# Kernel tuning notes

Hardware: AMD Instinct MI355X
Metric: run time of the kernel (lower is better)

Reference implementation:

```python
import jax, jax.numpy as jnp
import numpy as np

N_NODES = 40000
N_EDGES = 640000
D = 128
N_GRAPHS = 64


def gcn_conv(x, W, b, edge_index):
    """PyG-style GCNConv: add self-loops, symmetric norm, linear, scatter-add."""
    n = x.shape[0]
    loops = jnp.arange(n, dtype=edge_index.dtype)
    src = jnp.concatenate([edge_index[0], loops])  # message sources (x_j)
    dst = jnp.concatenate([edge_index[1], loops])  # aggregation targets
    # deg computed over targets (col) with unit edge weights, incl. self-loops
    deg = jax.ops.segment_sum(jnp.ones_like(src, dtype=x.dtype), dst, num_segments=n)
    dinv = jnp.where(deg > 0, jax.lax.rsqrt(jnp.maximum(deg, 1.0)), 0.0)
    norm = dinv[src] * dinv[dst]  # [E+N]
    h = x @ W  # [N, d_out]
    out = jax.ops.segment_sum(norm[:, None] * h[src], dst, num_segments=n)
    return out + b


def global_mean_pool(x, batch, num_graphs):
    summed = jax.ops.segment_sum(x, batch, num_segments=num_graphs)
    counts = jax.ops.segment_sum(jnp.ones((x.shape[0],), x.dtype), batch, num_segments=num_graphs)
    return summed / jnp.maximum(counts, 1.0)[:, None]


def setup_inputs() -> dict:
    key = jax.random.key(0)
    ks = jax.random.split(key, 6)
    x = jax.random.normal(ks[0], (N_NODES, D), dtype=jnp.float32)
    edge_index = jax.random.randint(ks[1], (2, N_EDGES), 0, N_NODES)
    batch = jnp.sort(jax.random.randint(ks[2], (N_NODES,), 0, N_GRAPHS))
    s = 1.0 / np.sqrt(D)
    W1 = jax.random.normal(ks[3], (D, D), dtype=jnp.float32) * s
    W2 = jax.random.normal(ks[4], (D, D), dtype=jnp.float32) * s
    b1 = jnp.zeros((D,), jnp.float32)
    b2 = jnp.zeros((D,), jnp.float32)
    return {"x": x, "edge_index": edge_index, "batch": batch,
            "W1": W1, "b1": b1, "W2": W2, "b2": b2}


def reference(x, edge_index, batch, W1, b1, W2, b2):
    h = jax.nn.relu(gcn_conv(x, W1, b1, edge_index))
    h = gcn_conv(h, W2, b2, edge_index)  # no ReLU on last layer
    return global_mean_pool(h, batch, N_GRAPHS)
```

## Files before the change

kernel.cpp:

```cpp
#include <hip/hip_runtime.h>

#define D 128
#define N_GRAPHS 64

typedef unsigned int uint32;
typedef __attribute__((ext_vector_type(8))) _Float16 f16x8;
typedef __attribute__((ext_vector_type(4))) float f32x4;

__device__ __forceinline__ float hl(uint32 u) {
    return (float)__builtin_bit_cast(_Float16, (unsigned short)(u & 0xFFFF));
}
__device__ __forceinline__ float hh(uint32 u) {
    return (float)__builtin_bit_cast(_Float16, (unsigned short)(u >> 16));
}
__device__ __forceinline__ uint32 h2pair(float a, float b) {
    unsigned short ua = __builtin_bit_cast(unsigned short, (_Float16)a);
    unsigned short ub = __builtin_bit_cast(unsigned short, (_Float16)b);
    return (uint32)ua | ((uint32)ub << 16);
}

__global__ __launch_bounds__(256) void prep_kernel(int* __restrict__ cnt,
                                                   const float* __restrict__ W1,
                                                   uint32* __restrict__ Wh, int n) {
    int i = blockIdx.x * 256 + threadIdx.x;
    if (i < n) {
        cnt[i] = 0;
    } else if (i < n + D * (D / 2)) {
        int j = i - n;
        int nn = j & 127, kd = j >> 7;
        float v0 = W1[(size_t)(2 * kd) * D + nn];
        float v1 = W1[(size_t)(2 * kd + 1) * D + nn];
        Wh[nn * 64 + kd] = h2pair(v0, v1);
    }
}


#define GBM 64

__global__ __launch_bounds__(256) void count_gemm_kernel(
    const float* __restrict__ A, const uint32* __restrict__ Wh,
    uint32* __restrict__ hb, int M, int gemmBlocks,
    const int* __restrict__ dst, int* __restrict__ cnt,
    int* __restrict__ rank, int E) {
    __shared__ uint32 lds[64 * 68];

    if (blockIdx.x >= gemmBlocks) {
        int e = (blockIdx.x - gemmBlocks) * 256 + threadIdx.x;
        if (e < E) rank[e] = atomicAdd(&cnt[dst[e]], 1);
        return;
    }

    uint32* As = lds;
    int tid = threadIdx.x;
    int row0 = blockIdx.x * GBM;

#pragma unroll
    for (int j = 0; j < 8; ++j) {
        int idx = tid + j * 256;
        int r = idx >> 5, c4 = idx & 31;
        float4 v = make_float4(0.f, 0.f, 0.f, 0.f);
        if (row0 + r < M) v = *(const float4*)&A[(size_t)(row0 + r) * D + c4 * 4];
        As[r * 68 + c4 * 2 + 0] = h2pair(v.x, v.y);
        As[r * 68 + c4 * 2 + 1] = h2pair(v.z, v.w);
    }
    __syncthreads();

    int wave = tid >> 6, lane = tid & 63;
    int quad = lane >> 4, l16 = lane & 15;
    int wr = (wave & 1) * 32;
    int wc = (wave >> 1) * 64;
    f32x4 acc[2][4];
#pragma unroll
    for (int mi = 0; mi < 2; ++mi)
#pragma unroll
        for (int ni = 0; ni < 4; ++ni) acc[mi][ni] = (f32x4){0.f, 0.f, 0.f, 0.f};

#pragma unroll
    for (int ks = 0; ks < 4; ++ks) {
        int kd = ks * 16 + quad * 4;
        f16x8 a0 = *(f16x8*)&As[(wr + l16) * 68 + kd];
        f16x8 a1 = *(f16x8*)&As[(wr + 16 + l16) * 68 + kd];
        f16x8 b0 = *(const f16x8*)&Wh[(wc + l16) * 64 + kd];
        f16x8 b1 = *(const f16x8*)&Wh[(wc + 16 + l16) * 64 + kd];
        f16x8 b2 = *(const f16x8*)&Wh[(wc + 32 + l16) * 64 + kd];
        f16x8 b3 = *(const f16x8*)&Wh[(wc + 48 + l16) * 64 + kd];
        acc[0][0] = __builtin_amdgcn_mfma_f32_16x16x32_f16(a0, b0, acc[0][0], 0, 0, 0);
        acc[0][1] = __builtin_amdgcn_mfma_f32_16x16x32_f16(a0, b1, acc[0][1], 0, 0, 0);
        acc[0][2] = __builtin_amdgcn_mfma_f32_16x16x32_f16(a0, b2, acc[0][2], 0, 0, 0);
        acc[0][3] = __builtin_amdgcn_mfma_f32_16x16x32_f16(a0, b3, acc[0][3], 0, 0, 0);
        acc[1][0] = __builtin_amdgcn_mfma_f32_16x16x32_f16(a1, b0, acc[1][0], 0, 0, 0);
        acc[1][1] = __builtin_amdgcn_mfma_f32_16x16x32_f16(a1, b1, acc[1][1], 0, 0, 0);
        acc[1][2] = __builtin_amdgcn_mfma_f32_16x16x32_f16(a1, b2, acc[1][2], 0, 0, 0);
        acc[1][3] = __builtin_amdgcn_mfma_f32_16x16x32_f16(a1, b3, acc[1][3], 0, 0, 0);
    }
    __syncthreads();

    unsigned short* cs = (unsigned short*)lds;
#pragma unroll
    for (int mi = 0; mi < 2; ++mi)
#pragma unroll
        for (int ni = 0; ni < 4; ++ni)
#pragma unroll
            for (int r = 0; r < 4; ++r) {
                int row = wr + mi * 16 + quad * 4 + r;
                int col2 = wc + ni * 16 + l16;
                cs[row * 128 + col2] =
                    __builtin_bit_cast(unsigned short, (_Float16)acc[mi][ni][r]);
            }
    __syncthreads();
#pragma unroll
    for (int j = 0; j < 4; ++j) {
        int idx = tid + j * 256;
        int r = idx >> 4, q = idx & 15;
        if (row0 + r < M)
            *(uint4*)&hb[(size_t)(row0 + r) * 64 + q * 4] = *(uint4*)&lds[r * 64 + q * 4];
    }
}


__global__ __launch_bounds__(1024) void scanA_kernel(const int* __restrict__ cnt,
                                                     int* __restrict__ rowptr,
                                                     int* __restrict__ tot,
                                                     float* __restrict__ dinv, int n) {
    __shared__ int swave[16];
    int t = threadIdx.x;
    int lane = t & 63, wave = t >> 6;
    int i = blockIdx.x * 1024 + t;
    int orig = (i < n) ? cnt[i] : 0;
    int v = orig;
#pragma unroll
    for (int off = 1; off < 64; off <<= 1) {
        int u = __shfl_up(v, off, 64);
        if (lane >= off) v += u;
    }
    if (lane == 63) swave[wave] = v;
    __syncthreads();
    if (wave == 0) {
        int wv = (lane < 16) ? swave[lane] : 0;
#pragma unroll
        for (int off = 1; off < 16; off <<= 1) {
            int u = __shfl_up(wv, off, 64);
            if (lane >= off) wv += u;
        }
        if (lane < 16) swave[lane] = wv;
    }
    if (i < n) dinv[i] = rsqrtf((float)(orig + 1));
    __syncthreads();
    int incl = v + ((wave > 0) ? swave[wave - 1] : 0);
    if (i < n) rowptr[i] = incl - orig;
    if (t == 1023) tot[blockIdx.x] = incl;
}

__global__ __launch_bounds__(1024) void scanB_kernel(int* __restrict__ rowptr,
                                                     const int* __restrict__ tot,
                                                     int n, int nchunks) {
    __shared__ int soff;
    int b = blockIdx.x, t = threadIdx.x;
    if (t == 0) {
        int o = 0;
        for (int j = 0; j < b; ++j) o += tot[j];
        soff = o;
    }
    __syncthreads();
    int i = b * 1024 + t;
    if (i < n) rowptr[i] += soff;
    if (b == 0 && t == 0) {
        int o = 0;
        for (int j = 0; j < nchunks; ++j) o += tot[j];
        rowptr[n] = o;
    }
}

__global__ void fill_kernel(const int* __restrict__ src, const int* __restrict__ dst,
                            const int* __restrict__ rowptr, const int* __restrict__ rank,
                            int* __restrict__ col, int E) {
    int e = blockIdx.x * blockDim.x + threadIdx.x;
    if (e < E) col[rowptr[dst[e]] + rank[e]] = src[e];
}


__global__ __launch_bounds__(128) void agg_kernel(const uint32* __restrict__ hb,
                                                  const int* __restrict__ rowptr,
                                                  const int* __restrict__ col,
                                                  const float* __restrict__ dinv,
                                                  const float* __restrict__ bias,
                                                  uint32* __restrict__ h1, int n) {
    int tid = threadIdx.x;
    int lane32 = tid & 31;
    int slot = tid >> 5;
    int node = blockIdx.x * 4 + slot;
    if (node >= n) return;
    const uint2* __restrict__ h2 = (const uint2*)hb;

    float di = dinv[node];
    float ws = di * di;
    uint2 su = h2[(size_t)node * 32 + lane32];
    float a0 = ws * hl(su.x), a1 = ws * hh(su.x);
    float a2 = ws * hl(su.y), a3 = ws * hh(su.y);

    int start = rowptr[node], end = rowptr[node + 1];
    for (int k = start; k < end; k += 8) {
        uint2 v[8];
        float w[8];
#pragma unroll
        for (int j = 0; j < 8; ++j) {
            int idx = k + j;
            int s = col[idx < end ? idx : start];
            w[j] = (idx < end) ? dinv[s] * di : 0.f;
            v[j] = h2[(size_t)s * 32 + lane32];
        }
#pragma unroll
        for (int j = 0; j < 8; ++j) {
            a0 = fmaf(w[j], hl(v[j].x), a0);
            a1 = fmaf(w[j], hh(v[j].x), a1);
            a2 = fmaf(w[j], hl(v[j].y), a2);
            a3 = fmaf(w[j], hh(v[j].y), a3);
        }
    }

    float4 b4 = ((const float4*)bias)[lane32];
    a0 = fmaxf(a0 + b4.x, 0.f);
    a1 = fmaxf(a1 + b4.y, 0.f);
    a2 = fmaxf(a2 + b4.z, 0.f);
    a3 = fmaxf(a3 + b4.w, 0.f);
    uint2 o;
    o.x = h2pair(a0, a1);
    o.y = h2pair(a2, a3);
    ((uint2*)h1)[(size_t)node * 32 + lane32] = o;
}


__global__ __launch_bounds__(128) void agg2_kernel(const uint32* __restrict__ h1,
                                                   const int* __restrict__ rowptr,
                                                   const int* __restrict__ col,
                                                   const float* __restrict__ dinv,
                                                   float* __restrict__ P2, int n) {
    int tid = threadIdx.x;
    int lane32 = tid & 31;
    int slot = tid >> 5;
    int node = blockIdx.x * 4 + slot;
    if (node >= n) return;
    const uint2* __restrict__ h2 = (const uint2*)h1;

    float di = dinv[node];
    float ws = di * di;
    uint2 su = h2[(size_t)node * 32 + lane32];
    float a0 = ws * hl(su.x), a1 = ws * hh(su.x);
    float a2 = ws * hl(su.y), a3 = ws * hh(su.y);

    int start = rowptr[node], end = rowptr[node + 1];
    for (int k = start; k < end; k += 8) {
        uint2 v[8];
        float w[8];
#pragma unroll
        for (int j = 0; j < 8; ++j) {
            int idx = k + j;
            int s = col[idx < end ? idx : start];
            w[j] = (idx < end) ? dinv[s] * di : 0.f;
            v[j] = h2[(size_t)s * 32 + lane32];
        }
#pragma unroll
        for (int j = 0; j < 8; ++j) {
            a0 = fmaf(w[j], hl(v[j].x), a0);
            a1 = fmaf(w[j], hh(v[j].x), a1);
            a2 = fmaf(w[j], hl(v[j].y), a2);
            a3 = fmaf(w[j], hh(v[j].y), a3);
        }
    }

    *(float4*)&P2[(size_t)node * D + lane32 * 4] = make_float4(a0, a1, a2, a3);
}

#define PSL 16

__global__ __launch_bounds__(128) void pool_kernel(const float* __restrict__ P2,
                                                   const int* __restrict__ batch,
                                                   float* __restrict__ Ppart, int n) {
    __shared__ int srange[2];
    int t = threadIdx.x;
    int g = blockIdx.x >> 4;
    int kslice = blockIdx.x & 15;
    if (t == 0) {
        int lo = 0, hi = n;
        while (lo < hi) { int mid = (lo + hi) >> 1; if (batch[mid] < g) lo = mid + 1; else hi = mid; }
        srange[0] = lo;
        int g1 = g + 1;
        lo = 0; hi = n;
        while (lo < hi) { int mid = (lo + hi) >> 1; if (batch[mid] < g1) lo = mid + 1; else hi = mid; }
        srange[1] = lo;
    }
    __syncthreads();
    int lb = srange[0], cntg = srange[1] - srange[0];
    int a = lb + (int)(((long long)cntg * kslice) >> 4);
    int b = lb + (int)(((long long)cntg * (kslice + 1)) >> 4);

    float s = 0.f;
    int node = a;
    for (; node + 4 <= b; node += 4) {
        float v0 = P2[(size_t)(node + 0) * D + t];
        float v1 = P2[(size_t)(node + 1) * D + t];
        float v2 = P2[(size_t)(node + 2) * D + t];
        float v3 = P2[(size_t)(node + 3) * D + t];
        s += (v0 + v1) + (v2 + v3);
    }
    for (; node < b; ++node) s += P2[(size_t)node * D + t];
    Ppart[(size_t)blockIdx.x * D + t] = s;
}

__global__ __launch_bounds__(256) void out_kernel(const float* __restrict__ Ppart,
                                                  const float* __restrict__ W2,
                                                  const float* __restrict__ b2,
                                                  const int* __restrict__ batch, int n,
                                                  float* __restrict__ out) {
    __shared__ float gs[D];
    __shared__ float part[2][D];
    __shared__ float srinv;
    int g = blockIdx.x, t = threadIdx.x;
    int f = t & 127, half = t >> 7;
    if (t == 0) {
        int lo = 0, hi = n;
        while (lo < hi) { int mid = (lo + hi) >> 1; if (batch[mid] < g) lo = mid + 1; else hi = mid; }
        int lb = lo;
        int g1 = g + 1;
        lo = 0; hi = n;
        while (lo < hi) { int mid = (lo + hi) >> 1; if (batch[mid] < g1) lo = mid + 1; else hi = mid; }
        int cg = lo - lb;
        srinv = (cg > 0) ? 1.0f / (float)cg : 0.0f;
    }
    float s = 0.f;
    int j0 = half * (PSL / 2);
#pragma unroll
    for (int j = j0; j < j0 + PSL / 2; ++j)
        s += Ppart[((size_t)g * PSL + j) * D + f];
    part[half][f] = s;
    __syncthreads();
    if (half == 0) gs[f] = part[0][f] + part[1][f];
    __syncthreads();
    float acc = 0.f;
    int k0 = half * (D / 2);
#pragma unroll 8
    for (int k = k0; k < k0 + D / 2; ++k) acc = fmaf(gs[k], W2[k * D + f], acc);
    part[half][f] = acc;
    __syncthreads();
    if (half == 0) {
        float a = part[0][f] + part[1][f];
        float r = srinv;
        out[g * D + f] = (r > 0.f) ? fmaf(a, r, b2[f]) : 0.f;
    }
}


extern "C" void kernel_launch(void* const* d_in, const int* in_sizes, int n_in,
                              void* d_out, int out_size, void* d_ws, size_t ws_size,
                              hipStream_t stream) {
    const float* x  = (const float*)d_in[0];
    const int*   ei = (const int*)d_in[1];
    const int*   batch = (const int*)d_in[2];
    const float* W1 = (const float*)d_in[3];
    const float* b1 = (const float*)d_in[4];
    const float* W2 = (const float*)d_in[5];
    const float* b2 = (const float*)d_in[6];
    float* out = (float*)d_out;

    const int n = in_sizes[2];
    const int E = in_sizes[1] / 2;
    const int* src = ei;
    const int* dst = ei + E;

    char* ws = (char*)d_ws;
    size_t off = 0;
    auto carve = [&](size_t bytes) {
        size_t o = off;
        off = (off + bytes + 255) & ~(size_t)255;
        return (void*)(ws + o);
    };
    int*    cnt    = (int*)carve((size_t)n * 4);
    int*    rowptr = (int*)carve((size_t)(n + 1) * 4);
    float*  dinv   = (float*)carve((size_t)n * 4);
    int*    col    = (int*)carve((size_t)E * 4);
    uint32* hb     = (uint32*)carve((size_t)n * D * 2);
    uint32* h1     = (uint32*)carve((size_t)n * D * 2);
    int*    tot    = (int*)carve(64 * 4);
    int*    rank   = (int*)carve((size_t)E * 4);
    uint32* Wh     = (uint32*)carve((size_t)D * (D / 2) * 4);
    float*  P2     = (float*)carve((size_t)n * D * 4);
    float*  Ppart  = (float*)hb;
    (void)ws_size;

    const int nchunks = (n + 1023) >> 10;

    prep_kernel<<<(n + D * (D / 2) + 255) / 256, 256, 0, stream>>>(cnt, W1, Wh, n);

    const int gemmBlocks = (n + GBM - 1) / GBM;
    const int countBlocks = (E + 255) / 256;
    count_gemm_kernel<<<gemmBlocks + countBlocks, 256, 0, stream>>>(
        x, Wh, hb, n, gemmBlocks, dst, cnt, rank, E);

    scanA_kernel<<<nchunks, 1024, 0, stream>>>(cnt, rowptr, tot, dinv, n);
    scanB_kernel<<<nchunks, 1024, 0, stream>>>(rowptr, tot, n, nchunks);
    fill_kernel<<<(E + 255) / 256, 256, 0, stream>>>(src, dst, rowptr, rank, col, E);

    agg_kernel<<<(n + 3) / 4, 128, 0, stream>>>(hb, rowptr, col, dinv, b1, h1, n);

    agg2_kernel<<<(n + 3) / 4, 128, 0, stream>>>(h1, rowptr, col, dinv, P2, n);
    pool_kernel<<<N_GRAPHS * PSL, 128, 0, stream>>>(P2, batch, Ppart, n);
    out_kernel<<<N_GRAPHS, 256, 0, stream>>>(Ppart, W2, b2, batch, n, out);
}
```

Measured before the change: 229.1 us.

## Pre-scale features by dinv to drop per-edge norm weights in aggregation

Symmetric normalization is factored out: the layer-1 features are pre-multiplied by dinv inside a merged scale+fill kernel, and layer-1 outputs are stored pre-scaled by dinv, so aggregation becomes a plain sum of gathered rows followed by one dinv multiply per node. This removes the per-edge dinv[src] gather and multiply. It also replaces the padded 8-wide loop, which used clamped and masked edges, with a full-chunk loop plus a scalar remainder loop. The trade-off is an extra read-modify-write pass over the fp16 features and an additional fp16 rounding of the scaled values.

```diff
diff --git a/kernel.cpp b/kernel.cpp
--- a/kernel.cpp
+++ b/kernel.cpp
@@ -171,11 +171,27 @@
     }
 }
 
-__global__ void fill_kernel(const int* __restrict__ src, const int* __restrict__ dst,
-                            const int* __restrict__ rowptr, const int* __restrict__ rank,
-                            int* __restrict__ col, int E) {
-    int e = blockIdx.x * blockDim.x + threadIdx.x;
-    if (e < E) col[rowptr[dst[e]] + rank[e]] = src[e];
+__global__ __launch_bounds__(256) void scale_fill_kernel(
+    uint32* __restrict__ hb, const float* __restrict__ dinv, int scaleBlocks, int n,
+    const int* __restrict__ src, const int* __restrict__ dst,
+    const int* __restrict__ rowptr, const int* __restrict__ rank,
+    int* __restrict__ col, int E) {
+    if (blockIdx.x >= scaleBlocks) {
+        int e = (blockIdx.x - scaleBlocks) * 256 + threadIdx.x;
+        if (e < E) col[rowptr[dst[e]] + rank[e]] = src[e];
+        return;
+    }
+    int idx = blockIdx.x * 256 + threadIdx.x;
+    if (idx < n * 16) {
+        int node = idx >> 4;
+        float dv = dinv[node];
+        uint4 v = ((uint4*)hb)[idx];
+        v.x = h2pair(dv * hl(v.x), dv * hh(v.x));
+        v.y = h2pair(dv * hl(v.y), dv * hh(v.y));
+        v.z = h2pair(dv * hl(v.z), dv * hh(v.z));
+        v.w = h2pair(dv * hl(v.w), dv * hh(v.w));
+        ((uint4*)hb)[idx] = v;
+    }
 }
 
 
@@ -193,39 +209,39 @@
     const uint2* __restrict__ h2 = (const uint2*)hb;
 
     float di = dinv[node];
-    float ws = di * di;
     uint2 su = h2[(size_t)node * 32 + lane32];
-    float a0 = ws * hl(su.x), a1 = ws * hh(su.x);
-    float a2 = ws * hl(su.y), a3 = ws * hh(su.y);
-
-    int start = rowptr[node], end = rowptr[node + 1];
-    for (int k = start; k < end; k += 8) {
+    float a0 = hl(su.x), a1 = hh(su.x);
+    float a2 = hl(su.y), a3 = hh(su.y);
+
+    int k = rowptr[node], end = rowptr[node + 1];
+    for (; k + 8 <= end; k += 8) {
         uint2 v[8];
-        float w[8];
+#pragma unroll
+        for (int j = 0; j < 8; ++j) v[j] = h2[(size_t)col[k + j] * 32 + lane32];
 #pragma unroll
         for (int j = 0; j < 8; ++j) {
-            int idx = k + j;
-            int s = col[idx < end ? idx : start];
-            w[j] = (idx < end) ? dinv[s] * di : 0.f;
-            v[j] = h2[(size_t)s * 32 + lane32];
+            a0 += hl(v[j].x);
+            a1 += hh(v[j].x);
+            a2 += hl(v[j].y);
+            a3 += hh(v[j].y);
         }
-#pragma unroll
-        for (int j = 0; j < 8; ++j) {
-            a0 = fmaf(w[j], hl(v[j].x), a0);
-            a1 = fmaf(w[j], hh(v[j].x), a1);
-            a2 = fmaf(w[j], hl(v[j].y), a2);
-            a3 = fmaf(w[j], hh(v[j].y), a3);
-        }
+    }
+    for (; k < end; ++k) {
+        uint2 v = h2[(size_t)col[k] * 32 + lane32];
+        a0 += hl(v.x);
+        a1 += hh(v.x);
+        a2 += hl(v.y);
+        a3 += hh(v.y);
     }
 
     float4 b4 = ((const float4*)bias)[lane32];
-    a0 = fmaxf(a0 + b4.x, 0.f);
-    a1 = fmaxf(a1 + b4.y, 0.f);
-    a2 = fmaxf(a2 + b4.z, 0.f);
-    a3 = fmaxf(a3 + b4.w, 0.f);
+    float r0 = fmaxf(fmaf(di, a0, b4.x), 0.f);
+    float r1 = fmaxf(fmaf(di, a1, b4.y), 0.f);
+    float r2 = fmaxf(fmaf(di, a2, b4.z), 0.f);
+    float r3 = fmaxf(fmaf(di, a3, b4.w), 0.f);
     uint2 o;
-    o.x = h2pair(a0, a1);
-    o.y = h2pair(a2, a3);
+    o.x = h2pair(di * r0, di * r1);
+    o.y = h2pair(di * r2, di * r3);
     ((uint2*)h1)[(size_t)node * 32 + lane32] = o;
 }
 
@@ -243,32 +259,33 @@
     const uint2* __restrict__ h2 = (const uint2*)h1;
 
     float di = dinv[node];
-    float ws = di * di;
     uint2 su = h2[(size_t)node * 32 + lane32];
-    float a0 = ws * hl(su.x), a1 = ws * hh(su.x);
-    float a2 = ws * hl(su.y), a3 = ws * hh(su.y);
-
-    int start = rowptr[node], end = rowptr[node + 1];
-    for (int k = start; k < end; k += 8) {
+    float a0 = hl(su.x), a1 = hh(su.x);
+    float a2 = hl(su.y), a3 = hh(su.y);
+
+    int k = rowptr[node], end = rowptr[node + 1];
+    for (; k + 8 <= end; k += 8) {
         uint2 v[8];
-        float w[8];
+#pragma unroll
+        for (int j = 0; j < 8; ++j) v[j] = h2[(size_t)col[k + j] * 32 + lane32];
 #pragma unroll
         for (int j = 0; j < 8; ++j) {
-            int idx = k + j;
-            int s = col[idx < end ? idx : start];
-            w[j] = (idx < end) ? dinv[s] * di : 0.f;
-            v[j] = h2[(size_t)s * 32 + lane32];
+            a0 += hl(v[j].x);
+            a1 += hh(v[j].x);
+            a2 += hl(v[j].y);
+            a3 += hh(v[j].y);
         }
-#pragma unroll
-        for (int j = 0; j < 8; ++j) {
-            a0 = fmaf(w[j], hl(v[j].x), a0);
-            a1 = fmaf(w[j], hh(v[j].x), a1);
-            a2 = fmaf(w[j], hl(v[j].y), a2);
-            a3 = fmaf(w[j], hh(v[j].y), a3);
-        }
-    }
-
-    *(float4*)&P2[(size_t)node * D + lane32 * 4] = make_float4(a0, a1, a2, a3);
+    }
+    for (; k < end; ++k) {
+        uint2 v = h2[(size_t)col[k] * 32 + lane32];
+        a0 += hl(v.x);
+        a1 += hh(v.x);
+        a2 += hl(v.y);
+        a3 += hh(v.y);
+    }
+
+    *(float4*)&P2[(size_t)node * D + lane32 * 4] =
+        make_float4(di * a0, di * a1, di * a2, di * a3);
 }
 
 #define PSL 16
@@ -398,7 +415,10 @@
 
     scanA_kernel<<<nchunks, 1024, 0, stream>>>(cnt, rowptr, tot, dinv, n);
     scanB_kernel<<<nchunks, 1024, 0, stream>>>(rowptr, tot, n, nchunks);
-    fill_kernel<<<(E + 255) / 256, 256, 0, stream>>>(src, dst, rowptr, rank, col, E);
+    const int scaleBlocks = (n * 16 + 255) / 256;
+    const int fillBlocks = (E + 255) / 256;
+    scale_fill_kernel<<<scaleBlocks + fillBlocks, 256, 0, stream>>>(
+        hb, dinv, scaleBlocks, n, src, dst, rowptr, rank, col, E);
 
     agg_kernel<<<(n + 3) / 4, 128, 0, stream>>>(hb, rowptr, col, dinv, b1, h1, n);
 
```

Result: faster. 195.1 us (-14.8%).
